# Performance work log

Measured on AMD Instinct MI355X. Metric: run time of the kernel, lower is better.

Reference implementation:

```python
import jax, jax.numpy as jnp
import numpy as np

BATCH, SEQ = 64, 64
D = 256            # model_dim (state = [h;c], each half = 128)
HALF = D // 2
VOCAB = 32000
MLP_DIM = 1024
NUM_CLASSES = 3


def setup_inputs() -> dict:
    key = jax.random.key(0)
    ks = jax.random.split(key, 12)
    s = lambda k, shp, fan: jax.random.normal(k, shp, jnp.float32) * (2.0 / fan) ** 0.5
    return {
        "sentences": jax.random.randint(ks[0], (BATCH, SEQ), 0, VOCAB, dtype=jnp.int64),
        "transitions": jnp.zeros((BATCH, 2 * SEQ - 2), dtype=jnp.int64),
        "emb": jax.random.normal(ks[1], (VOCAB, D), jnp.float32) * 0.1,
        "comp_W": s(ks[2], (2 * HALF, 5 * HALF), 2 * HALF),
        "comp_b": jnp.zeros((5 * HALF,), jnp.float32),
        "sel_w": s(ks[3], (D, 1), D),
        "sel_b": jnp.zeros((1,), jnp.float32),
        "mlp_w0": s(ks[4], (D, MLP_DIM), D),
        "mlp_b0": jnp.zeros((MLP_DIM,), jnp.float32),
        "mlp_w1": s(ks[5], (MLP_DIM, MLP_DIM), MLP_DIM),
        "mlp_b1": jnp.zeros((MLP_DIM,), jnp.float32),
        "cls_w": s(ks[6], (MLP_DIM, NUM_CLASSES), MLP_DIM),
        "cls_b": jnp.zeros((NUM_CLASSES,), jnp.float32),
    }


def _treelstm(left, right, comp_W, comp_b):
    # left/right: [B, L, D] state pairs = concat(h, c)
    hl, cl = left[..., :HALF], left[..., HALF:]
    hr, cr = right[..., :HALF], right[..., HALF:]
    a = jnp.concatenate([hl, hr], -1) @ comp_W + comp_b  # [B, L, 5*HALF]
    i, fl, fr, g, o = jnp.split(a, 5, axis=-1)
    c = (jax.nn.sigmoid(fl) * cl + jax.nn.sigmoid(fr) * cr
         + jax.nn.sigmoid(i) * jnp.tanh(g))
    h = jax.nn.sigmoid(o) * jnp.tanh(c)
    return jnp.concatenate([h, c], -1)  # [B, L, D]


def _pyramid(x, comp_W, comp_b, sel_w, sel_b):
    # x: [B, S, D] leaf states. Gated pyramid merge, eval mode (temperature=1).
    states = x
    for layer in range(SEQ - 1, 0, -1):
        left, right = states[:, :-1], states[:, 1:]      # [B, layer, D]
        comp = _treelstm(left, right, comp_W, comp_b)    # [B, layer, D]
        logits = (comp @ sel_w + sel_b)[..., 0]          # [B, layer]
        probs = jax.nn.softmax(logits, axis=-1)
        cs = jnp.cumsum(probs, axis=-1)
        copy_right = cs - probs                          # sum_{j<pos}
        rcs = jnp.flip(jnp.cumsum(jnp.flip(probs, -1), -1), -1)
        copy_left = rcs - probs                          # sum_{j>pos}
        states = (copy_left[..., None] * left
                  + copy_right[..., None] * right
                  + probs[..., None] * comp)
    return states[:, 0]  # [B, D]


def reference(sentences, transitions, emb, comp_W, comp_b, sel_w, sel_b,
              mlp_w0, mlp_b0, mlp_w1, mlp_b1, cls_w, cls_b):
    x = emb[sentences]                                   # [B, S, D]
    h = _pyramid(x, comp_W, comp_b, sel_w, sel_b)        # [B, D]
    z = jax.nn.relu(h @ mlp_w0 + mlp_b0)
    z = jax.nn.relu(z @ mlp_w1 + mlp_b1)
    return z @ cls_w + cls_b                             # [B, num_classes]
```

## Files before the change

kernel.cpp:

```cpp
#include <hip/hip_runtime.h>

#define SEQ 64

typedef _Float16 f16;
typedef _Float16 f16x8 __attribute__((ext_vector_type(8)));
typedef _Float16 f16x2 __attribute__((ext_vector_type(2)));
typedef float f32x4 __attribute__((ext_vector_type(4)));

__device__ __forceinline__ float sig_(float x) {
  return __builtin_amdgcn_rcpf(1.0f + __expf(-x));
}
__device__ __forceinline__ float tanh_(float x) {
  return 1.0f - 2.0f * __builtin_amdgcn_rcpf(1.0f + __expf(2.0f * x));
}

template<int CTRL, int RMASK>
__device__ __forceinline__ float dpp_add(float x) {
  const int t = __builtin_amdgcn_update_dpp(0, __float_as_int(x), CTRL, RMASK, 0xF, true);
  return x + __int_as_float(t);
}
template<int CTRL>
__device__ __forceinline__ float dpp_max(float x) {
  const int t = __builtin_amdgcn_update_dpp(0, __float_as_int(x), CTRL, 0xF, 0xF, true);
  return fmaxf(x, __int_as_float(t));
}
__device__ __forceinline__ float red16(float v) {
  v = dpp_add<0xB1, 0xF>(v);
  v = dpp_add<0x4E, 0xF>(v);
  v = dpp_add<0x124, 0xF>(v);
  v = dpp_add<0x128, 0xF>(v);
  return v;
}

__device__ __forceinline__ int hOff(int n, int f) {
  return n * 128 + ((((f >> 3) ^ (n & 15)) << 3) | (f & 7));
}

__device__ __forceinline__ f16x8 gatherB(const float* __restrict__ cW,
                                         int kk, int q, int wv, int quad, int l15) {
  const int col = (q * 8 + wv) * 16 + l15;
  const int kb  = kk * 32 + quad * 8;
  f16x8 v;
  #pragma unroll
  for (int j = 0; j < 8; ++j) v[j] = (f16)cW[(kb + j) * 640 + col];
  return v;
}

#define BLDS_OFF 0
#define CS_OFF   98304
#define HS_OFF   132624
#define LGP_OFF  149264
#define PS_OFF   151312
#define CLS_OFF  151568
#define CRS_OFF  151824
#define DYN_LDS  152080

__global__ __launch_bounds__(512, 1) void pyramid_kernel(
    const int*   __restrict__ sentences,
    const float* __restrict__ emb,
    const float* __restrict__ cW,
    const float* __restrict__ cb, const float* __restrict__ selw, const float* __restrict__ selb,
    const float* __restrict__ w0, const float* __restrict__ b0,
    const float* __restrict__ cbias,
    f16* __restrict__ z0h, float* __restrict__ out)
{
  extern __shared__ __align__(16) char dyn[];
  f16x8* Blds = (f16x8*)(dyn + BLDS_OFF);
  float* cS   = (float*)(dyn + CS_OFF);
  f16*   hS   = (f16*)  (dyn + HS_OFF);
  float* lgp  = (float*)(dyn + LGP_OFF);
  float* pS   = (float*)(dyn + PS_OFF);
  float* clS  = (float*)(dyn + CLS_OFF);
  float* crS  = (float*)(dyn + CRS_OFF);

  const int tid  = threadIdx.x;
  const int b    = blockIdx.x;
  const int wv   = tid >> 6;
  const int lane = tid & 63;
  const int quad = lane >> 4;
  const int l15  = lane & 15;
  const int d    = wv * 16 + l15;

  if (b == 0 && tid < 192) out[tid] = cbias[tid % 3];

  #pragma unroll
  for (int s = 0; s < 12; ++s) {
    const int kk = (s < 4) ? (4 + s) : (s - 4);
    const int q  = (s < 4) ? 3 : 4;
    Blds[s * 512 + tid] = gatherB(cW, kk, q, wv, quad, l15);
  }
  f16x8 Breg[28];
  #pragma unroll
  for (int kk = 0; kk < 8; ++kk)
    #pragma unroll
    for (int q = 0; q < 3; ++q)
      Breg[kk * 3 + q] = gatherB(cW, kk, q, wv, quad, l15);
  #pragma unroll
  for (int kk = 0; kk < 4; ++kk)
    Breg[24 + kk] = gatherB(cW, kk, 3, wv, quad, l15);

  {
    const int s = tid >> 3, part = tid & 7;
    const int row = sentences[b * SEQ + s];
    const float4* er = (const float4*)(emb + (size_t)row * 256 + part * 32);
    #pragma unroll
    for (int i4 = 0; i4 < 8; ++i4) {
      const float4 v = er[i4];
      const float vv[4] = {v.x, v.y, v.z, v.w};
      #pragma unroll
      for (int c = 0; c < 4; ++c) {
        const int f = part * 32 + i4 * 4 + c;
        if (f < 128) hS[hOff(s, f)] = (f16)vv[c];
        else         cS[s * 132 + (f - 128)] = vv[c];
      }
    }
  }
  if (tid < 128) hS[64 * 128 + tid] = (f16)0.f;
  if (tid < 132) cS[64 * 132 + tid] = 0.f;
  __syncthreads();

  float bq[5];
  #pragma unroll
  for (int q = 0; q < 5; ++q) bq[q] = cb[q * 128 + d];
  const float swh = selw[d], swc = selw[128 + d], selbv = selb[0];

  for (int W = 63; W >= 1; --W) {
    const int NMT = (W + 15) >> 4;
    float chF[4][4], ccF[4][4];

    #pragma unroll
    for (int mt = 0; mt < 4; ++mt) if (mt < NMT) {
      f32x4 acc[5];
      #pragma unroll
      for (int q = 0; q < 5; ++q) acc[q] = (f32x4){bq[q], bq[q], bq[q], bq[q]};
      #pragma unroll
      for (int kk = 0; kk < 8; ++kk) {
        const int n   = mt * 16 + l15 + (kk >> 2);
        const int blk = (kk & 3) * 4 + quad;
        const f16x8 av = *(const f16x8*)&hS[n * 128 + ((blk ^ (n & 15)) << 3)];
        #pragma unroll
        for (int q = 0; q < 3; ++q)
          acc[q] = __builtin_amdgcn_mfma_f32_16x16x32_f16(av, Breg[kk * 3 + q], acc[q], 0, 0, 0);
        const f16x8 b3 = (kk < 4) ? Breg[24 + kk] : Blds[(kk - 4) * 512 + tid];
        acc[3] = __builtin_amdgcn_mfma_f32_16x16x32_f16(av, b3, acc[3], 0, 0, 0);
        const f16x8 b4 = Blds[(4 + kk) * 512 + tid];
        acc[4] = __builtin_amdgcn_mfma_f32_16x16x32_f16(av, b4, acc[4], 0, 0, 0);
      }
      const int n0q = mt * 16 + quad * 4;
      float c5[5];
      #pragma unroll
      for (int r = 0; r < 5; ++r) c5[r] = cS[(n0q + r) * 132 + d];
      #pragma unroll
      for (int r = 0; r < 4; ++r) {
        const float c = sig_(acc[1][r]) * c5[r] + sig_(acc[2][r]) * c5[r + 1]
                      + sig_(acc[0][r]) * tanh_(acc[3][r]);
        const float h = sig_(acc[4][r]) * tanh_(c);
        ccF[mt][r] = c; chF[mt][r] = h;
        float v = red16(__builtin_fmaf(h, swh, c * swc));
        if (l15 == 0) {
          const int n = n0q + r;
          if (n < W) lgp[(wv << 6) + n] = v;
        }
      }
    }
    __syncthreads();

    {
      float lg = -3.0e38f;
      if (lane < W) {
        float s = selbv;
        #pragma unroll
        for (int dg = 0; dg < 8; ++dg) s += lgp[(dg << 6) + lane];
        lg = s;
      }
      float m = lg;
      m = dpp_max<0xB1>(m); m = dpp_max<0x4E>(m);
      m = dpp_max<0x124>(m); m = dpp_max<0x128>(m);
      m = fmaxf(m, __shfl_xor(m, 16, 64));
      m = fmaxf(m, __shfl_xor(m, 32, 64));
      const float e = (lane < W) ? __expf(lg - m) : 0.f;
      float t = e;
      t = dpp_add<0xB1, 0xF>(t); t = dpp_add<0x4E, 0xF>(t);
      t = dpp_add<0x124, 0xF>(t); t = dpp_add<0x128, 0xF>(t);
      t += __shfl_xor(t, 16, 64);
      t += __shfl_xor(t, 32, 64);
      const float p = e * __builtin_amdgcn_rcpf(t);
      float cs = p;
      cs = dpp_add<0x111, 0xF>(cs);
      cs = dpp_add<0x112, 0xF>(cs);
      cs = dpp_add<0x114, 0xF>(cs);
      cs = dpp_add<0x118, 0xF>(cs);
      cs = dpp_add<0x142, 0xA>(cs);
      cs = dpp_add<0x143, 0xC>(cs);
      const float T = __shfl(cs, 63, 64);
      if (lane < W) {
        pS[lane]  = p;
        clS[lane] = T - cs;
        crS[lane] = cs - p;
      }
    }

    #pragma unroll
    for (int mt = 0; mt < 4; ++mt) if (mt < NMT) {
      const int n0q = mt * 16 + quad * 4;
      const f32x4 pv  = *(const f32x4*)&pS[n0q];
      const f32x4 clv = *(const f32x4*)&clS[n0q];
      const f32x4 crv = *(const f32x4*)&crS[n0q];
      float oh[5], c5[5];
      #pragma unroll
      for (int r = 0; r < 5; ++r) {
        oh[r] = (float)hS[hOff(n0q + r, d)];
        c5[r] = cS[(n0q + r) * 132 + d];
      }
      #pragma unroll
      for (int r = 0; r < 4; ++r) {
        const int n = n0q + r;
        if (n < W) {
          const float nh = clv[r] * oh[r] + crv[r] * oh[r + 1] + pv[r] * chF[mt][r];
          const float nc = clv[r] * c5[r] + crv[r] * c5[r + 1] + pv[r] * ccF[mt][r];
          hS[hOff(n, d)] = (f16)nh;
          cS[n * 132 + d] = nc;
        }
      }
    }
    __syncthreads();
  }

  {
    const int c0 = 2 * tid;
    float a0 = 0.f, a1 = 0.f;
    #pragma unroll 8
    for (int k = 0; k < 128; ++k) {
      const float x  = (float)hS[k];
      const float2 w = *(const float2*)&w0[k * 1024 + c0];
      a0 = __builtin_fmaf(x, w.x, a0);
      a1 = __builtin_fmaf(x, w.y, a1);
    }
    #pragma unroll 8
    for (int k = 0; k < 128; ++k) {
      const float x  = cS[k];
      const float2 w = *(const float2*)&w0[(128 + k) * 1024 + c0];
      a0 = __builtin_fmaf(x, w.x, a0);
      a1 = __builtin_fmaf(x, w.y, a1);
    }
    f16x2 p;
    p[0] = (f16)fmaxf(a0 + b0[c0], 0.f);
    p[1] = (f16)fmaxf(a1 + b0[c0 + 1], 0.f);
    *(f16x2*)&z0h[b * 1024 + c0] = p;
  }
}

#define ZROW 264
__global__ __launch_bounds__(256) void z1_kernel(
    const f16* __restrict__ z0h, const float* __restrict__ w1,
    const float* __restrict__ b1, const float* __restrict__ cwt,
    float* __restrict__ out)
{
  __shared__ __align__(16) f16 ZL[64 * ZROW];
  __shared__ __align__(16) f16 WL[16 * ZROW];
  const int t    = threadIdx.x;
  const int wv   = t >> 6;
  const int lane = t & 63;
  const int quad = lane >> 4;
  const int l15  = lane & 15;
  const int c0   = blockIdx.x * 16;

  f32x4 acc = (f32x4){0.f, 0.f, 0.f, 0.f};
  for (int k0 = 0; k0 < 1024; k0 += 256) {
    __syncthreads();
    #pragma unroll
    for (int i = 0; i < 8; ++i) {
      const int idx8 = (t + i * 256) * 8;
      const int row  = idx8 >> 8;
      const int ko   = idx8 & 255;
      *(f16x8*)&ZL[row * ZROW + ko] = *(const f16x8*)&z0h[row * 1024 + k0 + ko];
    }
    #pragma unroll
    for (int i = 0; i < 16; ++i) {
      const int idx = t + i * 256;
      const int kc = idx >> 4, ci = idx & 15;
      WL[ci * ZROW + kc] = (f16)w1[(k0 + kc) * 1024 + c0 + ci];
    }
    __syncthreads();
    #pragma unroll
    for (int kk = 0; kk < 8; ++kk) {
      const f16x8 av = *(const f16x8*)&ZL[(wv * 16 + l15) * ZROW + kk * 32 + quad * 8];
      const f16x8 bv = *(const f16x8*)&WL[l15 * ZROW + kk * 32 + quad * 8];
      acc = __builtin_amdgcn_mfma_f32_16x16x32_f16(av, bv, acc, 0, 0, 0);
    }
  }

  const int col = c0 + l15;
  const float bias = b1[col];
  const float cw0 = cwt[col * 3], cw1 = cwt[col * 3 + 1], cw2 = cwt[col * 3 + 2];
  #pragma unroll
  for (int r = 0; r < 4; ++r) {
    const int row = wv * 16 + quad * 4 + r;
    const float z = fmaxf(acc[r] + bias, 0.f);
    const float p0 = red16(z * cw0);
    const float p1 = red16(z * cw1);
    const float p2 = red16(z * cw2);
    if (l15 == 0) {
      atomicAdd(&out[row * 3 + 0], p0);
      atomicAdd(&out[row * 3 + 1], p1);
      atomicAdd(&out[row * 3 + 2], p2);
    }
  }
}

extern "C" void kernel_launch(void* const* d_in, const int* in_sizes, int n_in,
                              void* d_out, int out_size, void* d_ws, size_t ws_size,
                              hipStream_t stream) {
  (void)in_sizes; (void)n_in; (void)out_size; (void)ws_size;
  f16* z0h = (f16*)d_ws;

  (void)hipFuncSetAttribute((const void*)pyramid_kernel,
                            hipFuncAttributeMaxDynamicSharedMemorySize, DYN_LDS);

  pyramid_kernel<<<dim3(64), dim3(512), DYN_LDS, stream>>>(
      (const int*)d_in[0],
      (const float*)d_in[2],
      (const float*)d_in[3],
      (const float*)d_in[4],
      (const float*)d_in[5],
      (const float*)d_in[6],
      (const float*)d_in[7],
      (const float*)d_in[8],
      (const float*)d_in[12],
      z0h, (float*)d_out);
  z1_kernel<<<dim3(64), dim3(256), 0, stream>>>(
      z0h,
      (const float*)d_in[9],
      (const float*)d_in[10],
      (const float*)d_in[11],
      (float*)d_out);
}
```

Measured before the change: 486.9 us.

## Fold log2e into gate weights, pad h rows, skip idle quads, use DPP reductions

```diff
diff --git a/kernel.cpp b/kernel.cpp
--- a/kernel.cpp
+++ b/kernel.cpp
@@ -1,17 +1,28 @@
 #include <hip/hip_runtime.h>
 
 #define SEQ 64
+#define LOG2E 1.4426950408889634f
 
 typedef _Float16 f16;
 typedef _Float16 f16x8 __attribute__((ext_vector_type(8)));
 typedef _Float16 f16x2 __attribute__((ext_vector_type(2)));
 typedef float f32x4 __attribute__((ext_vector_type(4)));
 
-__device__ __forceinline__ float sig_(float x) {
-  return __builtin_amdgcn_rcpf(1.0f + __expf(-x));
+__device__ __forceinline__ float exp2_(float x) {
+#if __has_builtin(__builtin_amdgcn_exp2f)
+  return __builtin_amdgcn_exp2f(x);
+#else
+  return __builtin_exp2f(x);
+#endif
+}
+__device__ __forceinline__ float sigp_(float a) {
+  return __builtin_amdgcn_rcpf(1.0f + exp2_(-a));
+}
+__device__ __forceinline__ float tanhp_(float a) {
+  return 1.0f - 2.0f * __builtin_amdgcn_rcpf(1.0f + exp2_(a));
 }
 __device__ __forceinline__ float tanh_(float x) {
-  return 1.0f - 2.0f * __builtin_amdgcn_rcpf(1.0f + __expf(2.0f * x));
+  return 1.0f - 2.0f * __builtin_amdgcn_rcpf(1.0f + exp2_(x * (2.0f * LOG2E)));
 }
 
 template<int CTRL, int RMASK>
@@ -31,29 +42,31 @@
   v = dpp_add<0x128, 0xF>(v);
   return v;
 }
-
-__device__ __forceinline__ int hOff(int n, int f) {
-  return n * 128 + ((((f >> 3) ^ (n & 15)) << 3) | (f & 7));
-}
+__device__ __forceinline__ float lane63f(float v) {
+  return __int_as_float(__builtin_amdgcn_readlane(__float_as_int(v), 63));
+}
+
+#define HROW 136
 
 __device__ __forceinline__ f16x8 gatherB(const float* __restrict__ cW,
-                                         int kk, int q, int wv, int quad, int l15) {
+                                         int kk, int q, int wv, int quad, int l15,
+                                         float sc) {
   const int col = (q * 8 + wv) * 16 + l15;
   const int kb  = kk * 32 + quad * 8;
   f16x8 v;
   #pragma unroll
-  for (int j = 0; j < 8; ++j) v[j] = (f16)cW[(kb + j) * 640 + col];
+  for (int j = 0; j < 8; ++j) v[j] = (f16)(cW[(kb + j) * 640 + col] * sc);
   return v;
 }
 
 #define BLDS_OFF 0
 #define CS_OFF   98304
 #define HS_OFF   132624
-#define LGP_OFF  149264
-#define PS_OFF   151312
-#define CLS_OFF  151568
-#define CRS_OFF  151824
-#define DYN_LDS  152080
+#define LGP_OFF  150304
+#define PS_OFF   152352
+#define CLS_OFF  152608
+#define CRS_OFF  152864
+#define DYN_LDS  153120
 
 __global__ __launch_bounds__(512, 1) void pyramid_kernel(
     const int*   __restrict__ sentences,
@@ -87,17 +100,18 @@
   for (int s = 0; s < 12; ++s) {
     const int kk = (s < 4) ? (4 + s) : (s - 4);
     const int q  = (s < 4) ? 3 : 4;
-    Blds[s * 512 + tid] = gatherB(cW, kk, q, wv, quad, l15);
+    const float sc = (q == 3) ? (2.0f * LOG2E) : LOG2E;
+    Blds[s * 512 + tid] = gatherB(cW, kk, q, wv, quad, l15, sc);
   }
   f16x8 Breg[28];
   #pragma unroll
   for (int kk = 0; kk < 8; ++kk)
     #pragma unroll
     for (int q = 0; q < 3; ++q)
-      Breg[kk * 3 + q] = gatherB(cW, kk, q, wv, quad, l15);
+      Breg[kk * 3 + q] = gatherB(cW, kk, q, wv, quad, l15, LOG2E);
   #pragma unroll
   for (int kk = 0; kk < 4; ++kk)
-    Breg[24 + kk] = gatherB(cW, kk, 3, wv, quad, l15);
+    Breg[24 + kk] = gatherB(cW, kk, 3, wv, quad, l15, 2.0f * LOG2E);
 
   {
     const int s = tid >> 3, part = tid & 7;
@@ -110,18 +124,19 @@
       #pragma unroll
       for (int c = 0; c < 4; ++c) {
         const int f = part * 32 + i4 * 4 + c;
-        if (f < 128) hS[hOff(s, f)] = (f16)vv[c];
+        if (f < 128) hS[s * HROW + f] = (f16)vv[c];
         else         cS[s * 132 + (f - 128)] = vv[c];
       }
     }
   }
-  if (tid < 128) hS[64 * 128 + tid] = (f16)0.f;
-  if (tid < 132) cS[64 * 132 + tid] = 0.f;
+  if (tid < HROW) hS[64 * HROW + tid] = (f16)0.f;
+  if (tid < 132)  cS[64 * 132 + tid] = 0.f;
   __syncthreads();
 
   float bq[5];
   #pragma unroll
-  for (int q = 0; q < 5; ++q) bq[q] = cb[q * 128 + d];
+  for (int q = 0; q < 5; ++q)
+    bq[q] = cb[q * 128 + d] * ((q == 3) ? (2.0f * LOG2E) : LOG2E);
   const float swh = selw[d], swc = selw[128 + d], selbv = selb[0];
 
   for (int W = 63; W >= 1; --W) {
@@ -133,11 +148,10 @@
       f32x4 acc[5];
       #pragma unroll
       for (int q = 0; q < 5; ++q) acc[q] = (f32x4){bq[q], bq[q], bq[q], bq[q]};
+      const int rb = (mt * 16 + l15) * HROW + quad * 8;
       #pragma unroll
       for (int kk = 0; kk < 8; ++kk) {
-        const int n   = mt * 16 + l15 + (kk >> 2);
-        const int blk = (kk & 3) * 4 + quad;
-        const f16x8 av = *(const f16x8*)&hS[n * 128 + ((blk ^ (n & 15)) << 3)];
+        const f16x8 av = *(const f16x8*)&hS[rb + (kk >> 2) * HROW + (kk & 3) * 32];
         #pragma unroll
         for (int q = 0; q < 3; ++q)
           acc[q] = __builtin_amdgcn_mfma_f32_16x16x32_f16(av, Breg[kk * 3 + q], acc[q], 0, 0, 0);
@@ -147,19 +161,21 @@
         acc[4] = __builtin_amdgcn_mfma_f32_16x16x32_f16(av, b4, acc[4], 0, 0, 0);
       }
       const int n0q = mt * 16 + quad * 4;
-      float c5[5];
-      #pragma unroll
-      for (int r = 0; r < 5; ++r) c5[r] = cS[(n0q + r) * 132 + d];
-      #pragma unroll
-      for (int r = 0; r < 4; ++r) {
-        const float c = sig_(acc[1][r]) * c5[r] + sig_(acc[2][r]) * c5[r + 1]
-                      + sig_(acc[0][r]) * tanh_(acc[3][r]);
-        const float h = sig_(acc[4][r]) * tanh_(c);
-        ccF[mt][r] = c; chF[mt][r] = h;
-        float v = red16(__builtin_fmaf(h, swh, c * swc));
-        if (l15 == 0) {
-          const int n = n0q + r;
-          if (n < W) lgp[(wv << 6) + n] = v;
+      if (n0q < W) {
+        float c5[5];
+        #pragma unroll
+        for (int r = 0; r < 5; ++r) c5[r] = cS[(n0q + r) * 132 + d];
+        #pragma unroll
+        for (int r = 0; r < 4; ++r) {
+          const float c = sigp_(acc[1][r]) * c5[r] + sigp_(acc[2][r]) * c5[r + 1]
+                        + sigp_(acc[0][r]) * tanhp_(acc[3][r]);
+          const float h = sigp_(acc[4][r]) * tanh_(c);
+          ccF[mt][r] = c; chF[mt][r] = h;
+          float v = red16(__builtin_fmaf(h, swh, c * swc));
+          if (l15 == 0) {
+            const int n = n0q + r;
+            if (n < W) lgp[(wv << 6) + n] = v;
+          }
         }
       }
     }
@@ -176,14 +192,14 @@
       float m = lg;
       m = dpp_max<0xB1>(m); m = dpp_max<0x4E>(m);
       m = dpp_max<0x124>(m); m = dpp_max<0x128>(m);
-      m = fmaxf(m, __shfl_xor(m, 16, 64));
-      m = fmaxf(m, __shfl_xor(m, 32, 64));
+      m = dpp_max<0x142>(m); m = dpp_max<0x143>(m);
+      m = lane63f(m);
       const float e = (lane < W) ? __expf(lg - m) : 0.f;
       float t = e;
       t = dpp_add<0xB1, 0xF>(t); t = dpp_add<0x4E, 0xF>(t);
       t = dpp_add<0x124, 0xF>(t); t = dpp_add<0x128, 0xF>(t);
-      t += __shfl_xor(t, 16, 64);
-      t += __shfl_xor(t, 32, 64);
+      t = dpp_add<0x142, 0xF>(t); t = dpp_add<0x143, 0xF>(t);
+      t = lane63f(t);
       const float p = e * __builtin_amdgcn_rcpf(t);
       float cs = p;
       cs = dpp_add<0x111, 0xF>(cs);
@@ -192,7 +208,7 @@
       cs = dpp_add<0x118, 0xF>(cs);
       cs = dpp_add<0x142, 0xA>(cs);
       cs = dpp_add<0x143, 0xC>(cs);
-      const float T = __shfl(cs, 63, 64);
+      const float T = lane63f(cs);
       if (lane < W) {
         pS[lane]  = p;
         clS[lane] = T - cs;
@@ -203,23 +219,25 @@
     #pragma unroll
     for (int mt = 0; mt < 4; ++mt) if (mt < NMT) {
       const int n0q = mt * 16 + quad * 4;
-      const f32x4 pv  = *(const f32x4*)&pS[n0q];
-      const f32x4 clv = *(const f32x4*)&clS[n0q];
-      const f32x4 crv = *(const f32x4*)&crS[n0q];
-      float oh[5], c5[5];
-      #pragma unroll
-      for (int r = 0; r < 5; ++r) {
-        oh[r] = (float)hS[hOff(n0q + r, d)];
-        c5[r] = cS[(n0q + r) * 132 + d];
-      }
-      #pragma unroll
-      for (int r = 0; r < 4; ++r) {
-        const int n = n0q + r;
-        if (n < W) {
-          const float nh = clv[r] * oh[r] + crv[r] * oh[r + 1] + pv[r] * chF[mt][r];
-          const float nc = clv[r] * c5[r] + crv[r] * c5[r + 1] + pv[r] * ccF[mt][r];
-          hS[hOff(n, d)] = (f16)nh;
-          cS[n * 132 + d] = nc;
+      if (n0q < W) {
+        const f32x4 pv  = *(const f32x4*)&pS[n0q];
+        const f32x4 clv = *(const f32x4*)&clS[n0q];
+        const f32x4 crv = *(const f32x4*)&crS[n0q];
+        float oh[5], c5[5];
+        #pragma unroll
+        for (int r = 0; r < 5; ++r) {
+          oh[r] = (float)hS[(n0q + r) * HROW + d];
+          c5[r] = cS[(n0q + r) * 132 + d];
+        }
+        #pragma unroll
+        for (int r = 0; r < 4; ++r) {
+          const int n = n0q + r;
+          if (n < W) {
+            const float nh = clv[r] * oh[r] + crv[r] * oh[r + 1] + pv[r] * chF[mt][r];
+            const float nc = clv[r] * c5[r] + crv[r] * c5[r + 1] + pv[r] * ccF[mt][r];
+            hS[n * HROW + d] = (f16)nh;
+            cS[n * 132 + d] = nc;
+          }
         }
       }
     }
```

Result: faster. 443.7 us (-8.9%).
